# Kernel optimization log

Hardware: AMD Instinct MI355X
Metric: run time of the kernel (lower is better)

## Reference

```python
import jax, jax.numpy as jnp
import numpy as np

B, T, V, D = 2048, 32, 1024, 256


def setup_inputs() -> dict:
    key = jax.random.key(0)
    k1, k2 = jax.random.split(key)
    input = jax.random.normal(k1, (B, T, D), dtype=jnp.float32)
    codebook = jax.random.normal(k2, (T, V, D), dtype=jnp.float32)
    return {"input": input, "codebook": codebook}


def reference(input, codebook):
    # input: [B, T, D]; codebook: [T, V, D]
    x = jnp.moveaxis(input, 1, 0)  # [T, B, D]
    # Squared euclidean distances; argmin is invariant to the sqrt in cdist.
    x2 = jnp.sum(x * x, axis=-1)[..., None]            # [T, B, 1]
    c2 = jnp.sum(codebook * codebook, axis=-1)[:, None, :]  # [T, 1, V]
    xc = jnp.einsum('tbd,tvd->tbv', x, codebook)       # [T, B, V]
    d2 = x2 - 2.0 * xc + c2                            # [T, B, V]
    idxes_ = jnp.argmin(d2, axis=-1)                   # [T, B]
    idxes = idxes_.T                                   # [B, T]
    # Direct per-token gather: embed[b, t] = codebook[t, idxes[b, t]]
    embed_ = codebook[jnp.arange(T)[:, None], idxes_]  # [T, B, D]
    embed = jnp.moveaxis(embed_, 0, 1)                 # [B, T, D]
    return embed, idxes
```

## Files before the change

### kernel.cpp

```cpp
#include <hip/hip_runtime.h>
#include <hip/hip_bf16.h>


#define B_ 2048
#define T_ 32
#define V_ 1024
#define D_ 256
#define BT 64
#define VTILE 256
#define NVT 4
#define CAP 32
#define MARGIN 8.0f

typedef __attribute__((ext_vector_type(8))) short short8;
typedef __attribute__((ext_vector_type(4))) float f32x4;

__device__ __forceinline__ unsigned short f2bf(float f) {
    unsigned u = __builtin_bit_cast(unsigned, f);
    unsigned r = u + 0x7FFFu + ((u >> 16) & 1u);
    return (unsigned short)(r >> 16);
}

__device__ __forceinline__ short8 pack8(float4 a, float4 b) {
    short8 r;
    r[0] = (short)f2bf(a.x); r[1] = (short)f2bf(a.y);
    r[2] = (short)f2bf(a.z); r[3] = (short)f2bf(a.w);
    r[4] = (short)f2bf(b.x); r[5] = (short)f2bf(b.y);
    r[6] = (short)f2bf(b.z); r[7] = (short)f2bf(b.w);
    return r;
}

__global__ void prep_kernel(const float* __restrict__ cb, float* __restrict__ c2,
                            unsigned short* __restrict__ cbb) {
    const int wave = threadIdx.x >> 6, lane = threadIdx.x & 63;
    const int row = blockIdx.x * 4 + wave;
    const float4 v4 = *(const float4*)(cb + (size_t)row * D_ + lane * 4);
    float s = v4.x * v4.x + v4.y * v4.y + v4.z * v4.z + v4.w * v4.w;
    #pragma unroll
    for (int off = 32; off; off >>= 1) s += __shfl_down(s, off, 64);
    if (lane == 0) c2[row] = s;

    ushort4 b4;
    b4.x = f2bf(v4.x); b4.y = f2bf(v4.y); b4.z = f2bf(v4.z); b4.w = f2bf(v4.w);
    *(ushort4*)(cbb + (size_t)row * D_ + lane * 4) = b4;
}

__global__ void c2_kernel(const float* __restrict__ cb, float* __restrict__ c2) {
    const int row = blockIdx.x * 4 + (threadIdx.x >> 6);
    const int lane = threadIdx.x & 63;
    const float4 v = ((const float4*)(cb + (size_t)row * D_))[lane];
    float s = v.x * v.x + v.y * v.y + v.z * v.z + v.w * v.w;
    #pragma unroll
    for (int off = 32; off; off >>= 1) s += __shfl_down(s, off, 64);
    if (lane == 0) c2[row] = s;
}

template<int USE_BF>
__global__ __launch_bounds__(256, 3)
void vq_kernel(const float* __restrict__ x, const float* __restrict__ cb,
               const float* __restrict__ c2, const unsigned short* __restrict__ cbb,
               float* __restrict__ out) {
    const int t  = blockIdx.x;
    const int b0 = blockIdx.y * BT;

    __shared__ short8 A_lds[BT * 32];
    __shared__ float  minPart4[BT][4];
    __shared__ unsigned rowCnt[BT];
    __shared__ unsigned short rowCand[BT * CAP];
    __shared__ unsigned short rowIdx[BT];

    const int tid = threadIdx.x;
    const int w = tid >> 6, lane = tid & 63;
    const int q = lane >> 4, ln = lane & 15;

    if (tid < BT) rowCnt[tid] = 0;
    ((float*)minPart4)[tid] = 3.4e38f;

    #pragma unroll
    for (int i = 0; i < 8; ++i) {
        int gid = i * 256 + tid, r = gid >> 5, g = gid & 31;
        const float4* src = (const float4*)(x + (((size_t)(b0 + r)) * T_ + t) * D_ + g * 8);
        A_lds[r * 32 + (g ^ (r & 15))] = pack8(src[0], src[1]);
    }

    const unsigned short* bb = cbb + ((size_t)t * V_ + w * 64 + ln) * D_ + q * 8;
    const float*          fb = cb  + ((size_t)t * V_ + w * 64 + ln) * D_ + q * 8;

    auto loadB = [&](int vt, int kc, short8 (&dst)[4]) {
        #pragma unroll
        for (int nt = 0; nt < 4; ++nt) {
            const int off = (vt * VTILE + nt * 16) * D_ + kc * 32;
            if constexpr (USE_BF) {
                dst[nt] = *(const short8*)(bb + off);
            } else {
                const float4* s = (const float4*)(fb + off);
                dst[nt] = pack8(s[0], s[1]);
            }
        }
    };

    short8 bufs0[4], bufs1[4];
    loadB(0, 0, bufs0);
    __syncthreads();

    for (int vt = 0; vt < NVT; ++vt) {
        f32x4 acc[4][4];
        #pragma unroll
        for (int mt = 0; mt < 4; ++mt)
            #pragma unroll
            for (int nt = 0; nt < 4; ++nt) acc[mt][nt] = (f32x4){0.f, 0.f, 0.f, 0.f};

        #pragma unroll
        for (int kc = 0; kc < 8; ++kc) {
            if (!(vt == NVT - 1 && kc == 7)) {
                if (kc & 1) loadB(vt + (kc == 7), (kc + 1) & 7, bufs0);
                else        loadB(vt,             kc + 1,       bufs1);
            }
            short8 af[4];
            #pragma unroll
            for (int mt = 0; mt < 4; ++mt)
                af[mt] = A_lds[(mt * 16 + ln) * 32 + ((kc * 4 + q) ^ ln)];
            #pragma unroll
            for (int mt = 0; mt < 4; ++mt)
                #pragma unroll
                for (int nt = 0; nt < 4; ++nt)
                    acc[mt][nt] = __builtin_amdgcn_mfma_f32_16x16x32_bf16(
                        af[mt], (kc & 1) ? bufs1[nt] : bufs0[nt], acc[mt][nt], 0, 0, 0);
        }

        const float* c2p = c2 + t * V_ + vt * VTILE + w * 64 + ln;
        float cc[4];
        #pragma unroll
        for (int nt = 0; nt < 4; ++nt) cc[nt] = c2p[nt * 16];

        #pragma unroll
        for (int mt = 0; mt < 4; ++mt)
            #pragma unroll
            for (int i = 0; i < 4; ++i) {
                float mn = 3.4e38f;
                #pragma unroll
                for (int nt = 0; nt < 4; ++nt)
                    mn = fminf(mn, fmaf(-2.0f, acc[mt][nt][i], cc[nt]));
                mn = fminf(mn, __shfl_xor(mn, 1, 64));
                mn = fminf(mn, __shfl_xor(mn, 2, 64));
                mn = fminf(mn, __shfl_xor(mn, 4, 64));
                mn = fminf(mn, __shfl_xor(mn, 8, 64));
                if (ln == 0) {
                    const int r = mt * 16 + q * 4 + i;
                    minPart4[r][w] = fminf(minPart4[r][w], mn);
                }
            }
        __syncthreads();

        #pragma unroll
        for (int mt = 0; mt < 4; ++mt)
            #pragma unroll
            for (int i = 0; i < 4; ++i) {
                const int r = mt * 16 + q * 4 + i;
                const float4 mp = *(const float4*)minPart4[r];
                const float thr = fminf(fminf(mp.x, mp.y), fminf(mp.z, mp.w)) + MARGIN;
                #pragma unroll
                for (int nt = 0; nt < 4; ++nt) {
                    float s = fmaf(-2.0f, acc[mt][nt][i], cc[nt]);
                    if (s < thr) {
                        unsigned pos = atomicAdd(&rowCnt[r], 1u);
                        if (pos < CAP)
                            rowCand[r * CAP + pos] =
                                (unsigned short)(vt * VTILE + w * 64 + nt * 16 + ln);
                    }
                }
            }
    }

    __syncthreads();
    const int grp = tid >> 4, l16 = tid & 15;
    #pragma unroll
    for (int j = 0; j < 4; ++j) {
        const int r = grp * 4 + j;
        const float* xp = x + (((size_t)(b0 + r)) * T_ + t) * D_ + l16 * 16;
        float4 xr[4];
        #pragma unroll
        for (int k = 0; k < 4; ++k) xr[k] = ((const float4*)xp)[k];

        const unsigned cnt = rowCnt[r];
        unsigned long long best = ~0ULL;
        auto score_v = [&](int v) {
            const float* cr = cb + ((size_t)t * V_ + v) * D_ + l16 * 16;
            float dot = 0.f;
            #pragma unroll
            for (int k = 0; k < 4; ++k) {
                float4 b = ((const float4*)cr)[k];
                dot = fmaf(xr[k].x, b.x, dot); dot = fmaf(xr[k].y, b.y, dot);
                dot = fmaf(xr[k].z, b.z, dot); dot = fmaf(xr[k].w, b.w, dot);
            }
            dot += __shfl_xor(dot, 1, 64);
            dot += __shfl_xor(dot, 2, 64);
            dot += __shfl_xor(dot, 4, 64);
            dot += __shfl_xor(dot, 8, 64);
            float sc = fmaf(-2.0f, dot, c2[t * V_ + v]);
            unsigned u = __builtin_bit_cast(unsigned, sc);
            u = (u & 0x80000000u) ? ~u : (u | 0x80000000u);
            unsigned long long e = ((unsigned long long)u << 32) | (unsigned)v;
            if (e < best) best = e;
        };
        if (cnt <= CAP) {
            for (unsigned c = 0; c < cnt; ++c) score_v((int)rowCand[r * CAP + c]);
        } else {
            for (int v = 0; v < V_; ++v) score_v(v);
        }
        if (l16 == 0) rowIdx[r] = (unsigned short)(best & 1023u);
    }
    __syncthreads();

    if (tid < BT)
        out[(size_t)B_ * T_ * D_ + (size_t)(b0 + tid) * T_ + t] = (float)rowIdx[tid];

    #pragma unroll
    for (int i = 0; i < 16; ++i) {
        const int row = w * 16 + i;
        const int idx = (int)rowIdx[row];
        const float4 src = *(const float4*)(cb + ((size_t)t * V_ + idx) * D_ + lane * 4);
        *(float4*)(out + (((size_t)(b0 + row)) * T_ + t) * D_ + lane * 4) = src;
    }
}

extern "C" void kernel_launch(void* const* d_in, const int* in_sizes, int n_in,
                              void* d_out, int out_size, void* d_ws, size_t ws_size,
                              hipStream_t stream) {
    const float* x  = (const float*)d_in[0];
    const float* cb = (const float*)d_in[1];
    float* out = (float*)d_out;
    float* c2  = (float*)d_ws;
    unsigned short* cbb = (unsigned short*)((char*)d_ws + 131072);
    const size_t NEED = 131072 + (size_t)T_ * V_ * D_ * 2;
    const int use_bf = (ws_size >= NEED) ? 1 : 0;

    if (use_bf) {
        prep_kernel<<<dim3(T_ * V_ / 4), 256, 0, stream>>>(cb, c2, cbb);
        vq_kernel<1><<<dim3(T_, B_ / BT), 256, 0, stream>>>(x, cb, c2, cbb, out);
    } else {
        c2_kernel<<<dim3(T_ * V_ / 4), 256, 0, stream>>>(cb, c2);
        vq_kernel<0><<<dim3(T_, B_ / BT), 256, 0, stream>>>(x, cb, c2, cbb, out);
    }
}
```

Measured before the change: 281.4 us.

## Split candidate rescoring and gather into a separate high-occupancy finish kernel

The main kernel no longer does the exact fp32 rescoring and gather. It writes each row's candidate count and packed candidate indices into that row's output embedding slot, and a new finish kernel (16 rows per block, launch bounds of 8) rescores the candidates, writes the index and overwrites the slot with the gathered codebook row. The goal is to take the serial, latency-bound rescoring tail out of the register-heavy MMA kernel and run it at higher occupancy. The prep kernel also processes four rows per wave, with a quarter of the blocks. The cost is an extra launch, and the output buffer is used as scratch, with a write and readback through global memory.

After: 273.1 us. 1.03x faster.

```diff
diff --git a/kernel.cpp b/kernel.cpp
--- a/kernel.cpp
+++ b/kernel.cpp
@@ -33,16 +33,31 @@
 __global__ void prep_kernel(const float* __restrict__ cb, float* __restrict__ c2,
                             unsigned short* __restrict__ cbb) {
     const int wave = threadIdx.x >> 6, lane = threadIdx.x & 63;
-    const int row = blockIdx.x * 4 + wave;
-    const float4 v4 = *(const float4*)(cb + (size_t)row * D_ + lane * 4);
-    float s = v4.x * v4.x + v4.y * v4.y + v4.z * v4.z + v4.w * v4.w;
-    #pragma unroll
-    for (int off = 32; off; off >>= 1) s += __shfl_down(s, off, 64);
-    if (lane == 0) c2[row] = s;
-
-    ushort4 b4;
-    b4.x = f2bf(v4.x); b4.y = f2bf(v4.y); b4.z = f2bf(v4.z); b4.w = f2bf(v4.w);
-    *(ushort4*)(cbb + (size_t)row * D_ + lane * 4) = b4;
+    const int row0 = blockIdx.x * 16 + wave * 4;
+    float4 v4[4];
+    float s[4];
+    #pragma unroll
+    for (int j = 0; j < 4; ++j) {
+        v4[j] = *(const float4*)(cb + (size_t)(row0 + j) * D_ + lane * 4);
+        s[j] = v4[j].x * v4[j].x + v4[j].y * v4[j].y
+             + v4[j].z * v4[j].z + v4[j].w * v4[j].w;
+    }
+    #pragma unroll
+    for (int off = 32; off; off >>= 1) {
+        #pragma unroll
+        for (int j = 0; j < 4; ++j) s[j] += __shfl_down(s[j], off, 64);
+    }
+    if (lane == 0) {
+        #pragma unroll
+        for (int j = 0; j < 4; ++j) c2[row0 + j] = s[j];
+    }
+    #pragma unroll
+    for (int j = 0; j < 4; ++j) {
+        ushort4 b4;
+        b4.x = f2bf(v4[j].x); b4.y = f2bf(v4[j].y);
+        b4.z = f2bf(v4[j].z); b4.w = f2bf(v4[j].w);
+        *(ushort4*)(cbb + (size_t)(row0 + j) * D_ + lane * 4) = b4;
+    }
 }
 
 __global__ void c2_kernel(const float* __restrict__ cb, float* __restrict__ c2) {
@@ -57,9 +72,9 @@
 
 template<int USE_BF>
 __global__ __launch_bounds__(256, 3)
-void vq_kernel(const float* __restrict__ x, const float* __restrict__ cb,
-               const float* __restrict__ c2, const unsigned short* __restrict__ cbb,
-               float* __restrict__ out) {
+void main_kernel(const float* __restrict__ x, const float* __restrict__ cb,
+                 const float* __restrict__ c2, const unsigned short* __restrict__ cbb,
+                 float* __restrict__ out) {
     const int t  = blockIdx.x;
     const int b0 = blockIdx.y * BT;
 
@@ -67,7 +82,6 @@
     __shared__ float  minPart4[BT][4];
     __shared__ unsigned rowCnt[BT];
     __shared__ unsigned short rowCand[BT * CAP];
-    __shared__ unsigned short rowIdx[BT];
 
     const int tid = threadIdx.x;
     const int w = tid >> 6, lane = tid & 63;
@@ -173,55 +187,69 @@
     }
 
     __syncthreads();
-    const int grp = tid >> 4, l16 = tid & 15;
-    #pragma unroll
-    for (int j = 0; j < 4; ++j) {
-        const int r = grp * 4 + j;
-        const float* xp = x + (((size_t)(b0 + r)) * T_ + t) * D_ + l16 * 16;
-        float4 xr[4];
-        #pragma unroll
-        for (int k = 0; k < 4; ++k) xr[k] = ((const float4*)xp)[k];
-
-        const unsigned cnt = rowCnt[r];
-        unsigned long long best = ~0ULL;
-        auto score_v = [&](int v) {
-            const float* cr = cb + ((size_t)t * V_ + v) * D_ + l16 * 16;
-            float dot = 0.f;
-            #pragma unroll
-            for (int k = 0; k < 4; ++k) {
-                float4 b = ((const float4*)cr)[k];
-                dot = fmaf(xr[k].x, b.x, dot); dot = fmaf(xr[k].y, b.y, dot);
-                dot = fmaf(xr[k].z, b.z, dot); dot = fmaf(xr[k].w, b.w, dot);
-            }
-            dot += __shfl_xor(dot, 1, 64);
-            dot += __shfl_xor(dot, 2, 64);
-            dot += __shfl_xor(dot, 4, 64);
-            dot += __shfl_xor(dot, 8, 64);
-            float sc = fmaf(-2.0f, dot, c2[t * V_ + v]);
-            unsigned u = __builtin_bit_cast(unsigned, sc);
-            u = (u & 0x80000000u) ? ~u : (u | 0x80000000u);
-            unsigned long long e = ((unsigned long long)u << 32) | (unsigned)v;
-            if (e < best) best = e;
-        };
-        if (cnt <= CAP) {
-            for (unsigned c = 0; c < cnt; ++c) score_v((int)rowCand[r * CAP + c]);
-        } else {
-            for (int v = 0; v < V_; ++v) score_v(v);
-        }
-        if (l16 == 0) rowIdx[r] = (unsigned short)(best & 1023u);
-    }
-    __syncthreads();
-
-    if (tid < BT)
-        out[(size_t)B_ * T_ * D_ + (size_t)(b0 + tid) * T_ + t] = (float)rowIdx[tid];
-
-    #pragma unroll
-    for (int i = 0; i < 16; ++i) {
-        const int row = w * 16 + i;
-        const int idx = (int)rowIdx[row];
-        const float4 src = *(const float4*)(cb + ((size_t)t * V_ + idx) * D_ + lane * 4);
-        *(float4*)(out + (((size_t)(b0 + row)) * T_ + t) * D_ + lane * 4) = src;
-    }
+    if (tid < BT) {
+        const int r = tid;
+        unsigned* slot = (unsigned*)(out + (((size_t)(b0 + r)) * T_ + t) * D_);
+        slot[0] = rowCnt[r];
+        const unsigned short* rc = &rowCand[r * CAP];
+        #pragma unroll
+        for (int k = 0; k < CAP / 2; ++k)
+            slot[1 + k] = (unsigned)rc[2 * k] | ((unsigned)rc[2 * k + 1] << 16);
+    }
+}
+
+__global__ __launch_bounds__(256, 8)
+void finish_kernel(const float* __restrict__ x, const float* __restrict__ cb,
+                   const float* __restrict__ c2, float* __restrict__ out) {
+    const int t = blockIdx.x;
+    const int b = blockIdx.y * 16 + (threadIdx.x >> 4);
+    const int l16 = threadIdx.x & 15;
+
+    float* slot = out + ((size_t)b * T_ + t) * D_;
+    const unsigned cnt = ((const unsigned*)slot)[0];
+
+    const float* xp = x + ((size_t)b * T_ + t) * D_ + l16 * 16;
+    float4 xr[4];
+    #pragma unroll
+    for (int k = 0; k < 4; ++k) xr[k] = ((const float4*)xp)[k];
+
+    unsigned long long best = ~0ULL;
+    auto score_v = [&](int v) {
+        const float* cr = cb + ((size_t)t * V_ + v) * D_ + l16 * 16;
+        float dot = 0.f;
+        #pragma unroll
+        for (int k = 0; k < 4; ++k) {
+            float4 bv = ((const float4*)cr)[k];
+            dot = fmaf(xr[k].x, bv.x, dot); dot = fmaf(xr[k].y, bv.y, dot);
+            dot = fmaf(xr[k].z, bv.z, dot); dot = fmaf(xr[k].w, bv.w, dot);
+        }
+        dot += __shfl_xor(dot, 1, 64);
+        dot += __shfl_xor(dot, 2, 64);
+        dot += __shfl_xor(dot, 4, 64);
+        dot += __shfl_xor(dot, 8, 64);
+        float sc = fmaf(-2.0f, dot, c2[t * V_ + v]);
+        unsigned u = __builtin_bit_cast(unsigned, sc);
+        u = (u & 0x80000000u) ? ~u : (u | 0x80000000u);
+        unsigned long long e = ((unsigned long long)u << 32) | (unsigned)v;
+        if (e < best) best = e;
+    };
+
+    if (cnt <= CAP) {
+        for (unsigned c = 0; c < cnt; ++c) {
+            unsigned pr = ((const unsigned*)slot)[1 + (c >> 1)];
+            score_v((int)((pr >> (16 * (c & 1))) & 0xffffu));
+        }
+    } else {
+        for (int v = 0; v < V_; ++v) score_v(v);
+    }
+
+    const int idx = (int)(best & 1023u);
+    if (l16 == 0) out[(size_t)B_ * T_ * D_ + (size_t)b * T_ + t] = (float)idx;
+
+    const float* cr = cb + ((size_t)t * V_ + idx) * D_;
+    #pragma unroll
+    for (int k = 0; k < 4; ++k)
+        *(float4*)(slot + k * 64 + l16 * 4) = *(const float4*)(cr + k * 64 + l16 * 4);
 }
 
 extern "C" void kernel_launch(void* const* d_in, const int* in_sizes, int n_in,
@@ -236,10 +264,11 @@
     const int use_bf = (ws_size >= NEED) ? 1 : 0;
 
     if (use_bf) {
-        prep_kernel<<<dim3(T_ * V_ / 4), 256, 0, stream>>>(cb, c2, cbb);
-        vq_kernel<1><<<dim3(T_, B_ / BT), 256, 0, stream>>>(x, cb, c2, cbb, out);
+        prep_kernel<<<dim3(T_ * V_ / 16), 256, 0, stream>>>(cb, c2, cbb);
+        main_kernel<1><<<dim3(T_, B_ / BT), 256, 0, stream>>>(x, cb, c2, cbb, out);
     } else {
         c2_kernel<<<dim3(T_ * V_ / 4), 256, 0, stream>>>(cb, c2);
-        vq_kernel<0><<<dim3(T_, B_ / BT), 256, 0, stream>>>(x, cb, c2, cbb, out);
-    }
-}
+        main_kernel<0><<<dim3(T_, B_ / BT), 256, 0, stream>>>(x, cb, c2, cbb, out);
+    }
+    finish_kernel<<<dim3(T_, B_ / 16), 256, 0, stream>>>(x, cb, c2, out);
+}
```
